# Kernel tuning notes

Hardware: AMD Instinct MI355X
Metric: run time of the kernel (lower is better)

## Reference

```python
import jax, jax.numpy as jnp
import numpy as np


def fwht(x):
    """Unnormalized fast Walsh-Hadamard transform over a 1-D vector (len = power of 2).
    Matches the torch chunk/cat stage ordering (MSB-first butterfly)."""
    n = x.shape[0]
    ll = int(round(np.log2(n)))
    for ii in range(ll):
        x = x.reshape(2 ** ii, 2, -1)
        x = jnp.concatenate([x[:, :1] + x[:, 1:], x[:, :1] - x[:, 1:]], axis=1)
    return x.reshape(n)


@jax.custom_vjp
def fwht_ff(x):
    # mirrors torch FastWalshHadamard.apply: plain FWHT forward,
    # backward = FWHT(grad) / sqrt(n) (as defined in the original autograd Function)
    return fwht(x)

def _fwht_ff_fwd(x):
    scale = jnp.asarray(1.0 / np.sqrt(float(x.shape[0])), x.dtype)
    return fwht(x), scale

def _fwht_ff_bwd(scale, g):
    return (scale * fwht(g),)

fwht_ff.defvjp(_fwht_ff_fwd, _fwht_ff_bwd)


def fastfood(theta, BB, Pi, GG, DD):
    """Fastfood projection of theta (dim dd) to DD dims using fixed vars."""
    LL = BB.shape[0]
    dd = theta.shape[0]
    k = min(dd, LL)  # F.pad with negative pad truncates; replicate that
    xx = jnp.zeros(LL, theta.dtype).at[:k].set(theta[:k])
    m2 = fwht(BB * xx)          # H B x
    m4 = m2[Pi] * GG            # G Pi H B x
    m5 = fwht_ff(m4)            # H G Pi H B x
    divisor = jnp.sqrt(LL * jnp.sum(GG * GG))
    return m5[:DD] / (divisor * np.sqrt(float(DD) / LL))


def _mk_ff_vars(key, DD):
    ll = int(np.ceil(np.log2(DD)))
    LL = 2 ** ll
    k1, k2, k3 = jax.random.split(key, 3)
    BB = jax.random.randint(k1, (LL,), 0, 2).astype(jnp.float32) * 2.0 - 1.0
    Pi = jax.random.permutation(k2, LL).astype(jnp.int32)
    GG = jax.random.normal(k3, (LL,), dtype=jnp.float32)
    return BB, Pi, GG


D_IN, D_HID, D_OUT = 768, 3072, 768
INTRINSIC = 2048
BATCH = 256


def setup_inputs() -> dict:
    key = jax.random.key(0)
    ks = jax.random.split(key, 12)
    x = jax.random.normal(ks[0], (BATCH, D_IN), dtype=jnp.float32)
    # original initializes intrinsic_parameter to zeros; use small randn so the
    # Fastfood path contributes non-trivially to the output for testing
    theta = jax.random.normal(ks[1], (INTRINSIC,), dtype=jnp.float32) * 0.01
    init_W1 = jax.random.normal(ks[2], (D_HID, D_IN), dtype=jnp.float32) * 0.02
    init_b1 = jax.random.normal(ks[3], (D_HID,), dtype=jnp.float32) * 0.02
    init_W2 = jax.random.normal(ks[4], (D_OUT, D_HID), dtype=jnp.float32) * 0.02
    init_b2 = jax.random.normal(ks[5], (D_OUT,), dtype=jnp.float32) * 0.02
    BB_W1, Pi_W1, GG_W1 = _mk_ff_vars(ks[6], D_HID * D_IN)
    BB_b1, Pi_b1, GG_b1 = _mk_ff_vars(ks[7], D_HID)
    BB_W2, Pi_W2, GG_W2 = _mk_ff_vars(ks[8], D_OUT * D_HID)
    BB_b2, Pi_b2, GG_b2 = _mk_ff_vars(ks[9], D_OUT)
    return {
        'x': x, 'theta': theta,
        'init_W1': init_W1, 'init_b1': init_b1, 'init_W2': init_W2, 'init_b2': init_b2,
        'BB_W1': BB_W1, 'Pi_W1': Pi_W1, 'GG_W1': GG_W1,
        'BB_b1': BB_b1, 'Pi_b1': Pi_b1, 'GG_b1': GG_b1,
        'BB_W2': BB_W2, 'Pi_W2': Pi_W2, 'GG_W2': GG_W2,
        'BB_b2': BB_b2, 'Pi_b2': Pi_b2, 'GG_b2': GG_b2,
    }


def reference(x, theta, init_W1, init_b1, init_W2, init_b2,
              BB_W1, Pi_W1, GG_W1, BB_b1, Pi_b1, GG_b1,
              BB_W2, Pi_W2, GG_W2, BB_b2, Pi_b2, GG_b2):
    # param = initial_value + fastfood(theta) for every wrapped parameter
    W1 = init_W1 + fastfood(theta, BB_W1, Pi_W1, GG_W1, init_W1.size).reshape(init_W1.shape)
    b1 = init_b1 + fastfood(theta, BB_b1, Pi_b1, GG_b1, init_b1.size)
    W2 = init_W2 + fastfood(theta, BB_W2, Pi_W2, GG_W2, init_W2.size).reshape(init_W2.shape)
    b2 = init_b2 + fastfood(theta, BB_b2, Pi_b2, GG_b2, init_b2.size)
    # wrapped module forward: Linear -> ReLU -> Linear
    h = jax.nn.relu(x @ W1.T + b1)
    return h @ W2.T + b2
```

## Files before the change

kernel.cpp:

```cpp
#include <hip/hip_runtime.h>
#include <hip/hip_bf16.h>

typedef __attribute__((ext_vector_type(8))) short bf16x8;
typedef __attribute__((ext_vector_type(8))) unsigned short u16x8;
typedef __attribute__((ext_vector_type(4))) float f32x4;

template <int N, int S>
__device__ __forceinline__ void reg_fwht(float* v) {
#pragma unroll
  for (int h = 1; h < N; h <<= 1)
#pragma unroll
    for (int g = 0; g < N; g += 2 * h)
#pragma unroll
      for (int j = 0; j < h; ++j) {
        float a = v[(g + j) * S], b = v[(g + j + h) * S];
        v[(g + j) * S] = a + b;
        v[(g + j + h) * S] = a - b;
      }
}

__device__ __forceinline__ unsigned short f2bf(float f) {
  unsigned u = __float_as_uint(f);
  unsigned r = (u + 0x7fff + ((u >> 16) & 1)) >> 16;
  return (unsigned short)r;
}

__device__ __forceinline__ void lds_fwht(float* s, int n, int tid, int T) {
  for (int h = 1; h < n; h <<= 1) {
    __syncthreads();
    for (int t = tid; t < (n >> 1); t += T) {
      int i0 = ((t & ~(h - 1)) << 1) | (t & (h - 1));
      int i1 = i0 + h;
      float a = s[i0], b = s[i1];
      s[i0] = a + b;
      s[i1] = a - b;
    }
  }
  __syncthreads();
}

__device__ __forceinline__ void fwht2048_block(float w[8], float* pad,
                                               float* dst, int t) {
  reg_fwht<8, 1>(w);
#pragma unroll
  for (int j = 0; j < 8; ++j) {
    int i = t + 256 * j;
    pad[i + 4 * (i >> 5)] = w[j];
  }
  __syncthreads();
  {
    int base = 8 * t + 4 * (t >> 2);
    float4 a = *(float4*)(pad + base);
    float4 b = *(float4*)(pad + base + 4);
    float u[8] = {a.x, a.y, a.z, a.w, b.x, b.y, b.z, b.w};
    reg_fwht<8, 1>(u);
    *(float4*)(pad + base) = make_float4(u[0], u[1], u[2], u[3]);
    *(float4*)(pad + base + 4) = make_float4(u[4], u[5], u[6], u[7]);
  }
  __syncthreads();
  {
    int b0 = (t & 7) + 64 * (t >> 3);
    float u[8];
#pragma unroll
    for (int j = 0; j < 8; ++j) {
      int i = b0 + 8 * j;
      u[j] = pad[i + 4 * (i >> 5)];
    }
    reg_fwht<8, 1>(u);
#pragma unroll
    for (int j = 0; j < 8; ++j) {
      int i = b0 + 8 * j;
      pad[i + 4 * (i >> 5)] = u[j];
    }
  }
  __syncthreads();
#pragma unroll
  for (int g = 0; g < 2; ++g) {
    int b0 = (t & 63) + 256 * ((g << 2) | (t >> 6));
    float u[4];
#pragma unroll
    for (int j = 0; j < 4; ++j) {
      int i = b0 + 64 * j;
      u[j] = pad[i + 4 * (i >> 5)];
    }
    reg_fwht<4, 1>(u);
#pragma unroll
    for (int j = 0; j < 4; ++j) dst[b0 + 64 * j] = u[j];
  }
  __syncthreads();
}

__global__ __launch_bounds__(256) void k_pre(
    const float* __restrict__ theta, const float* __restrict__ BB0,
    const float* __restrict__ BB1, float* __restrict__ m2s,
    const float* __restrict__ x, __hip_bfloat16* __restrict__ xb) {
  __shared__ __align__(16) float pad[2304];
  int b = blockIdx.x, t = threadIdx.x;
  if (b < 2) {
    const float* BB = b ? BB1 : BB0;
    float w[8];
#pragma unroll
    for (int j = 0; j < 8; ++j) {
      int i = t + 256 * j;
      w[j] = BB[i] * theta[i];
    }
    fwht2048_block(w, pad, m2s + b * 2048, t);
  } else {
    int id0 = (b - 2) * 256 + t;
#pragma unroll
    for (int it = 0; it < 2; ++it) {
      int id = id0 + it * 24576;
      float4 xv = ((const float4*)x)[id];
      ushort4 o;
      o.x = f2bf(xv.x);
      o.y = f2bf(xv.y);
      o.z = f2bf(xv.z);
      o.w = f2bf(xv.w);
      ((ushort4*)xb)[id] = o;
    }
  }
}

#define LLW 4194304

__global__ __launch_bounds__(256) void k_front(
    const int* __restrict__ Pi1, const float* __restrict__ GG1,
    const int* __restrict__ Pi2, const float* __restrict__ GG2,
    const float* __restrict__ m2s, unsigned short* __restrict__ m4b,
    float* __restrict__ partial, const float* __restrict__ theta,
    const float* __restrict__ BBb1, const int* __restrict__ Pib1,
    const float* __restrict__ GGb1, const float* __restrict__ ib1,
    float* __restrict__ b1w, const float* __restrict__ BBb2,
    const int* __restrict__ Pib2, const float* __restrict__ GGb2,
    const float* __restrict__ ib2, float* __restrict__ b2w) {
  __shared__ __align__(16) float s[9216];
  __shared__ float red[4];
  int b = blockIdx.x, t = threadIdx.x;

  if (b >= 2) {
    int bb = b - 2;
    int pipe = bb >> 9, chunk = bb & 511;
    const int* Pi = pipe ? Pi2 : Pi1;
    const float* GG = pipe ? GG2 : GG1;
    const float* mm = m2s + pipe * 2048;
    for (int u = t; u < 512; u += 256) ((float4*)s)[u] = ((const float4*)mm)[u];
    __syncthreads();

    long base = (long)chunk * 8192;
    const int4* p4 = (const int4*)(Pi + base);
    const float4* g4 = (const float4*)(GG + base);
    float v[32];
    float lsum = 0.f;
#pragma unroll
    for (int j = 0; j < 8; ++j) {
      int4 p = p4[t + j * 256];
      float4 g = g4[t + j * 256];
      lsum += g.x * g.x + g.y * g.y + g.z * g.z + g.w * g.w;
      v[j * 4 + 0] = s[p.x & 2047] * g.x;
      v[j * 4 + 1] = s[p.y & 2047] * g.y;
      v[j * 4 + 2] = s[p.z & 2047] * g.z;
      v[j * 4 + 3] = s[p.w & 2047] * g.w;
    }
    for (int off = 32; off; off >>= 1) lsum += __shfl_down(lsum, off, 64);
    if ((t & 63) == 0) red[t >> 6] = lsum;

#pragma unroll
    for (int e = 0; e < 4; ++e) reg_fwht<8, 4>(v + e);

    __syncthreads();
    if (t == 0) partial[pipe * 512 + chunk] = red[0] + red[1] + red[2] + red[3];

#pragma unroll
    for (int j = 0; j < 8; ++j) {
      int A = t * 4 + 4 * (t >> 3) + j * 1152;
      *(float4*)(s + A) =
          make_float4(v[j * 4], v[j * 4 + 1], v[j * 4 + 2], v[j * 4 + 3]);
    }
    __syncthreads();
    {
      int b0 = (t & 31) + (t >> 5) * 1024;
      float w[32];
#pragma unroll
      for (int j2 = 0; j2 < 32; ++j2) {
        int i = b0 + j2 * 32;
        w[j2] = s[i + 4 * (i >> 5)];
      }
      reg_fwht<32, 1>(w);
#pragma unroll
      for (int j2 = 0; j2 < 32; ++j2) {
        int i = b0 + j2 * 32;
        s[i + 4 * (i >> 5)] = w[j2];
      }
    }
    __syncthreads();
#pragma unroll
    for (int q = 0; q < 8; ++q) {
      float4 r = *(const float4*)(s + t * 36 + q * 4);
      v[q * 4 + 0] = r.x;
      v[q * 4 + 1] = r.y;
      v[q * 4 + 2] = r.z;
      v[q * 4 + 3] = r.w;
    }
    reg_fwht<32, 1>(v);
    unsigned short* o = m4b + (long)pipe * LLW + base + t * 32;
#pragma unroll
    for (int q = 0; q < 4; ++q) {
      u16x8 pk;
#pragma unroll
      for (int e = 0; e < 8; ++e) pk[e] = f2bf(v[q * 8 + e]);
      *(u16x8*)(o + q * 8) = pk;
    }
  } else if (b == 0) {
    float* tabd = s + 6144;
    float w[8];
#pragma unroll
    for (int j = 0; j < 8; ++j) {
      int i = t + 256 * j;
      w[j] = BBb1[i] * theta[i];
    }
    fwht2048_block(w, s, tabd, t);

    float w16[16];
    float lsum = 0.f;
#pragma unroll
    for (int j = 0; j < 16; ++j) {
      int i = t + 256 * j;
      float g = GGb1[i];
      lsum += g * g;
      w16[j] = tabd[Pib1[i] & 2047] * g;
    }
    reg_fwht<16, 1>(w16);
#pragma unroll
    for (int j = 0; j < 16; ++j) {
      int i = t + 256 * j;
      s[i + 4 * (i >> 5)] = w16[j];
    }
    for (int off = 32; off; off >>= 1) lsum += __shfl_down(lsum, off, 64);
    if ((t & 63) == 0) s[4608 + (t >> 6)] = lsum;
    __syncthreads();
    float S = s[4608] + s[4609] + s[4610] + s[4611];
    {
      int base16 = 16 * t + 4 * (t >> 1);
      float u[16];
#pragma unroll
      for (int q = 0; q < 4; ++q) {
        float4 r = *(float4*)(s + base16 + q * 4);
        u[q * 4 + 0] = r.x;
        u[q * 4 + 1] = r.y;
        u[q * 4 + 2] = r.z;
        u[q * 4 + 3] = r.w;
      }
      reg_fwht<16, 1>(u);
#pragma unroll
      for (int q = 0; q < 4; ++q)
        *(float4*)(s + base16 + q * 4) =
            make_float4(u[q * 4], u[q * 4 + 1], u[q * 4 + 2], u[q * 4 + 3]);
    }
    __syncthreads();
    {
      float scale = 1.0f / sqrtf(S * 3072.0f);
      int b0 = (t & 15) + 256 * (t >> 4);
      float u[16];
#pragma unroll
      for (int j = 0; j < 16; ++j) {
        int i = b0 + 16 * j;
        u[j] = s[i + 4 * (i >> 5)];
      }
      reg_fwht<16, 1>(u);
#pragma unroll
      for (int j = 0; j < 16; ++j) {
        int i = b0 + 16 * j;
        if (i < 3072) b1w[i] = ib1[i] + u[j] * scale;
      }
    }
  } else {
    float* tab2 = s;
    float* m42 = s + 1024;
    for (int i = t; i < 1024; i += 256) tab2[i] = BBb2[i] * theta[i];
    lds_fwht(tab2, 1024, t, 256);
    float lsum = 0.f;
    for (int i = t; i < 1024; i += 256) {
      float g = GGb2[i];
      lsum += g * g;
      m42[i] = tab2[Pib2[i] & 1023] * g;
    }
    for (int off = 32; off; off >>= 1) lsum += __shfl_down(lsum, off, 64);
    if ((t & 63) == 0) s[2048 + (t >> 6)] = lsum;
    lds_fwht(m42, 1024, t, 256);
    float S = s[2048] + s[2049] + s[2050] + s[2051];
    float scale = 1.0f / sqrtf(S * 768.0f);
    for (int i = t; i < 768; i += 256) b2w[i] = ib2[i] + m42[i] * scale;
  }
}

__global__ __launch_bounds__(256) void k_f2c(
    const unsigned short* __restrict__ m4b, const float* __restrict__ iW1,
    const float* __restrict__ iW2, const float* __restrict__ partial,
    __hip_bfloat16* __restrict__ W1b, __hip_bfloat16* __restrict__ W2b) {
  __shared__ __align__(16) float s[10480];
  __shared__ float red[4];
  int b = blockIdx.x, t = threadIdx.x;
  int pipe = b >> 9;
  int l0 = (b & 511) * 16;
  const unsigned short* mp = m4b + (long)pipe * LLW;
  const float* initW = pipe ? iW2 : iW1;
  unsigned short* outW = (unsigned short*)(pipe ? W2b : W1b);

  {
    float ps = partial[pipe * 512 + t] + partial[pipe * 512 + 256 + t];
    for (int off = 32; off; off >>= 1) ps += __shfl_down(ps, off, 64);
    if ((t & 63) == 0) red[t >> 6] = ps;
  }

#pragma unroll
  for (int u = 0; u < 4; ++u) {
    int idx = t + u * 256;
    int r = idx >> 1, h8 = (idx & 1) * 8;
    u16x8 raw = *(const u16x8*)(mp + (long)r * 8192 + l0 + h8);
    float* dp = s + r * 20 + (r >> 5) * 16 + h8;
    float4 f0, f1v;
    f0.x = __uint_as_float((unsigned)raw[0] << 16);
    f0.y = __uint_as_float((unsigned)raw[1] << 16);
    f0.z = __uint_as_float((unsigned)raw[2] << 16);
    f0.w = __uint_as_float((unsigned)raw[3] << 16);
    f1v.x = __uint_as_float((unsigned)raw[4] << 16);
    f1v.y = __uint_as_float((unsigned)raw[5] << 16);
    f1v.z = __uint_as_float((unsigned)raw[6] << 16);
    f1v.w = __uint_as_float((unsigned)raw[7] << 16);
    *(float4*)dp = f0;
    *(float4*)(dp + 4) = f1v;
  }
  __syncthreads();

  {
    int c = t & 15, rg = t >> 4;
    float w[32];
#pragma unroll
    for (int j = 0; j < 32; ++j) {
      int r = rg * 32 + j;
      w[j] = s[r * 20 + (r >> 5) * 16 + c];
    }
    reg_fwht<32, 1>(w);
#pragma unroll
    for (int j = 0; j < 32; ++j) {
      int r = rg * 32 + j;
      s[r * 20 + (r >> 5) * 16 + c] = w[j];
    }
  }
  __syncthreads();

  {
    int c = t & 15;
    float w[32];
#pragma unroll
    for (int k = 0; k < 2; ++k) {
      int b0 = (t >> 4) * 2 + k;
#pragma unroll
      for (int j4 = 0; j4 < 16; ++j4) {
        int r = b0 + 32 * j4;
        w[k * 16 + j4] = s[r * 20 + (r >> 5) * 16 + c];
      }
      reg_fwht<16, 1>(w + k * 16);
#pragma unroll
      for (int j4 = 0; j4 < 16; ++j4) {
        int r = b0 + 32 * j4;
        s[r * 20 + (r >> 5) * 16 + c] = w[k * 16 + j4];
      }
    }
  }
  __syncthreads();

  float S = red[0] + red[1] + red[2] + red[3];
  float scale = 1.0f / sqrtf(S * 2359296.0f);
#pragma unroll
  for (int u = 0; u < 5; ++u) {
    int idx = t + u * 256;
    if (idx < 1152) {
      int r = idx >> 2, c4 = (idx & 3) * 4;
      const float* sp = s + r * 20 + (r >> 5) * 16 + c4;
      long gi = (long)r * 8192 + l0 + c4;
      float4 iv = *(const float4*)(initW + gi);
      ushort4 pk;
      pk.x = f2bf(iv.x + sp[0] * scale);
      pk.y = f2bf(iv.y + sp[1] * scale);
      pk.z = f2bf(iv.z + sp[2] * scale);
      pk.w = f2bf(iv.w + sp[3] * scale);
      *(ushort4*)(outW + gi) = pk;
    }
  }
}

template <int NACC, int KCH, bool RELU, bool OUT_BF16>
__global__ __launch_bounds__(256) void k_gemm(
    const __hip_bfloat16* __restrict__ A, const __hip_bfloat16* __restrict__ B,
    const float* __restrict__ bias, void* __restrict__ C, int M, int N, int K) {
  int wid = blockIdx.x * 4 + (threadIdx.x >> 6);
  int lane = threadIdx.x & 63;
  int ntiles = N / (16 * NACC);
  int mt = wid / ntiles, nt = wid % ntiles;
  if (mt * 16 >= M) return;
  int ml = lane & 15;
  int q = lane >> 4;
  const short* As = (const short*)A;
  const short* Bs = (const short*)B;
  long arow = (long)(mt * 16 + ml) * K + q * 8;
  int KH = K / KCH;
  f32x4 acc[KCH][NACC] = {};
  for (int k = 0; k < KH; k += 32) {
#pragma unroll
    for (int c = 0; c < KCH; ++c) {
      bf16x8 av = *(const bf16x8*)(As + arow + k + c * KH);
#pragma unroll
      for (int a = 0; a < NACC; ++a) {
        int n = nt * 16 * NACC + a * 16 + ml;
        bf16x8 bv = *(const bf16x8*)(Bs + (long)n * K + q * 8 + k + c * KH);
        acc[c][a] =
            __builtin_amdgcn_mfma_f32_16x16x32_bf16(av, bv, acc[c][a], 0, 0, 0);
      }
    }
  }
#pragma unroll
  for (int a = 0; a < NACC; ++a) {
    int n = nt * 16 * NACC + a * 16 + ml;
    float bv = bias[n];
#pragma unroll
    for (int r = 0; r < 4; ++r) {
      float vv = bv;
#pragma unroll
      for (int c = 0; c < KCH; ++c) vv += acc[c][a][r];
      int mm = mt * 16 + q * 4 + r;
      if (RELU) vv = fmaxf(vv, 0.f);
      if (OUT_BF16)
        ((__hip_bfloat16*)C)[(long)mm * N + n] = __float2bfloat16(vv);
      else
        ((float*)C)[(long)mm * N + n] = vv;
    }
  }
}

#define OFF_PART 0
#define OFF_M2S 4096
#define OFF_M4B (OFF_M2S + 16384)
#define OFF_W1B (OFF_M4B + 2 * LLW * 2)
#define OFF_W2B (OFF_W1B + 4718592)
#define OFF_HB (OFF_W2B + 4718592)
#define OFF_XB (OFF_HB + 1572864)
#define OFF_B1 (OFF_XB + 393216)
#define OFF_B2 (OFF_B1 + 12288)

extern "C" void kernel_launch(void* const* d_in, const int* in_sizes, int n_in,
                              void* d_out, int out_size, void* d_ws,
                              size_t ws_size, hipStream_t stream) {
  const float* x = (const float*)d_in[0];
  const float* theta = (const float*)d_in[1];
  const float* iW1 = (const float*)d_in[2];
  const float* ib1 = (const float*)d_in[3];
  const float* iW2 = (const float*)d_in[4];
  const float* ib2 = (const float*)d_in[5];
  const float* BB_W1 = (const float*)d_in[6];
  const int* Pi_W1 = (const int*)d_in[7];
  const float* GG_W1 = (const float*)d_in[8];
  const float* BB_b1 = (const float*)d_in[9];
  const int* Pi_b1 = (const int*)d_in[10];
  const float* GG_b1 = (const float*)d_in[11];
  const float* BB_W2 = (const float*)d_in[12];
  const int* Pi_W2 = (const int*)d_in[13];
  const float* GG_W2 = (const float*)d_in[14];
  const float* BB_b2 = (const float*)d_in[15];
  const int* Pi_b2 = (const int*)d_in[16];
  const float* GG_b2 = (const float*)d_in[17];

  char* ws = (char*)d_ws;
  float* partial = (float*)(ws + OFF_PART);
  float* m2s = (float*)(ws + OFF_M2S);
  unsigned short* m4b = (unsigned short*)(ws + OFF_M4B);
  __hip_bfloat16* W1b = (__hip_bfloat16*)(ws + OFF_W1B);
  __hip_bfloat16* W2b = (__hip_bfloat16*)(ws + OFF_W2B);
  __hip_bfloat16* hb = (__hip_bfloat16*)(ws + OFF_HB);
  __hip_bfloat16* xb = (__hip_bfloat16*)(ws + OFF_XB);
  float* b1w = (float*)(ws + OFF_B1);
  float* b2w = (float*)(ws + OFF_B2);

  k_pre<<<98, 256, 0, stream>>>(theta, BB_W1, BB_W2, m2s, x, xb);
  k_front<<<1026, 256, 0, stream>>>(Pi_W1, GG_W1, Pi_W2, GG_W2, m2s, m4b,
                                    partial, theta, BB_b1, Pi_b1, GG_b1, ib1,
                                    b1w, BB_b2, Pi_b2, GG_b2, ib2, b2w);
  k_f2c<<<1024, 256, 0, stream>>>(m4b, iW1, iW2, partial, W1b, W2b);
  k_gemm<2, 1, true, true><<<384, 256, 0, stream>>>(xb, W1b, b1w, hb, 256,
                                                    3072, 768);
  k_gemm<1, 2, false, false><<<192, 256, 0, stream>>>(hb, W2b, b2w, d_out, 256,
                                                      768, 3072);
}
```

Before: 226.9 us.

## Transpose m4b intermediate layout and split-K GEMMs across waves with LDS reduction

The front kernel now writes the bf16 FWHT intermediate in a layout where each f2c block reads one contiguous 8192-element segment, and f2c remaps block indices to match. This turns strided gathers into coalesced reads at the cost of strided writes in the producer. Both GEMMs switch from per-wave in-register K chunking to split-K across waves within a block, reduced through shared memory. This doubles or quadruples the number of blocks for more parallelism, but adds a __syncthreads and LDS traffic.

```diff
diff --git a/kernel.cpp b/kernel.cpp
--- a/kernel.cpp
+++ b/kernel.cpp
@@ -202,13 +202,14 @@
       v[q * 4 + 3] = r.w;
     }
     reg_fwht<32, 1>(v);
-    unsigned short* o = m4b + (long)pipe * LLW + base + t * 32;
+    unsigned short* o = m4b + (long)pipe * LLW;
+    long a0 = (long)(2 * t) * 8192 + (long)chunk * 16;
 #pragma unroll
     for (int q = 0; q < 4; ++q) {
       u16x8 pk;
 #pragma unroll
       for (int e = 0; e < 8; ++e) pk[e] = f2bf(v[q * 8 + e]);
-      *(u16x8*)(o + q * 8) = pk;
+      *(u16x8*)(o + a0 + (q >> 1) * 8192 + (q & 1) * 8) = pk;
     }
   } else if (b == 0) {
     float* tabd = s + 6144;
@@ -301,8 +302,10 @@
   __shared__ float red[4];
   int b = blockIdx.x, t = threadIdx.x;
   int pipe = b >> 9;
-  int l0 = (b & 511) * 16;
-  const unsigned short* mp = m4b + (long)pipe * LLW;
+  int lb = b & 511;
+  int g = ((lb & 7) << 6) | (lb >> 3);
+  int l0 = g * 16;
+  const unsigned short* mp = m4b + (long)pipe * LLW + (long)g * 8192;
   const float* initW = pipe ? iW2 : iW1;
   unsigned short* outW = (unsigned short*)(pipe ? W2b : W1b);
 
@@ -313,11 +316,10 @@
   }
 
 #pragma unroll
-  for (int u = 0; u < 4; ++u) {
-    int idx = t + u * 256;
-    int r = idx >> 1, h8 = (idx & 1) * 8;
-    u16x8 raw = *(const u16x8*)(mp + (long)r * 8192 + l0 + h8);
-    float* dp = s + r * 20 + (r >> 5) * 16 + h8;
+  for (int q = 0; q < 4; ++q) {
+    u16x8 raw = *(const u16x8*)(mp + t * 32 + q * 8);
+    int r = 2 * t + (q >> 1), cb = (q & 1) * 8;
+    float* dp = s + r * 20 + (r >> 5) * 16 + cb;
     float4 f0, f1v;
     f0.x = __uint_as_float((unsigned)raw[0] << 16);
     f0.y = __uint_as_float((unsigned)raw[1] << 16);
@@ -390,50 +392,56 @@
   }
 }
 
-template <int NACC, int KCH, bool RELU, bool OUT_BF16>
+template <int NACC, int SPLITK, bool RELU, bool OUT_BF16>
 __global__ __launch_bounds__(256) void k_gemm(
     const __hip_bfloat16* __restrict__ A, const __hip_bfloat16* __restrict__ B,
     const float* __restrict__ bias, void* __restrict__ C, int M, int N, int K) {
-  int wid = blockIdx.x * 4 + (threadIdx.x >> 6);
-  int lane = threadIdx.x & 63;
+  __shared__ float red[4 * NACC * 320];
+  int wave = threadIdx.x >> 6, lane = threadIdx.x & 63;
+  int tileid = blockIdx.x * (4 / SPLITK) + wave / SPLITK;
+  int sk = wave % SPLITK;
   int ntiles = N / (16 * NACC);
-  int mt = wid / ntiles, nt = wid % ntiles;
-  if (mt * 16 >= M) return;
+  int mt = tileid / ntiles, nt = tileid % ntiles;
   int ml = lane & 15;
   int q = lane >> 4;
   const short* As = (const short*)A;
   const short* Bs = (const short*)B;
   long arow = (long)(mt * 16 + ml) * K + q * 8;
-  int KH = K / KCH;
-  f32x4 acc[KCH][NACC] = {};
-  for (int k = 0; k < KH; k += 32) {
-#pragma unroll
-    for (int c = 0; c < KCH; ++c) {
-      bf16x8 av = *(const bf16x8*)(As + arow + k + c * KH);
-#pragma unroll
-      for (int a = 0; a < NACC; ++a) {
-        int n = nt * 16 * NACC + a * 16 + ml;
-        bf16x8 bv = *(const bf16x8*)(Bs + (long)n * K + q * 8 + k + c * KH);
-        acc[c][a] =
-            __builtin_amdgcn_mfma_f32_16x16x32_bf16(av, bv, acc[c][a], 0, 0, 0);
-      }
-    }
-  }
-#pragma unroll
-  for (int a = 0; a < NACC; ++a) {
-    int n = nt * 16 * NACC + a * 16 + ml;
-    float bv = bias[n];
-#pragma unroll
-    for (int r = 0; r < 4; ++r) {
-      float vv = bv;
-#pragma unroll
-      for (int c = 0; c < KCH; ++c) vv += acc[c][a][r];
-      int mm = mt * 16 + q * 4 + r;
-      if (RELU) vv = fmaxf(vv, 0.f);
-      if (OUT_BF16)
-        ((__hip_bfloat16*)C)[(long)mm * N + n] = __float2bfloat16(vv);
-      else
-        ((float*)C)[(long)mm * N + n] = vv;
+  int KS = K / SPLITK, k0 = sk * KS;
+  f32x4 acc[NACC] = {};
+  for (int k = k0; k < k0 + KS; k += 32) {
+    bf16x8 av = *(const bf16x8*)(As + arow + k);
+#pragma unroll
+    for (int a = 0; a < NACC; ++a) {
+      int n = nt * 16 * NACC + a * 16 + ml;
+      bf16x8 bv = *(const bf16x8*)(Bs + (long)n * K + q * 8 + k);
+      acc[a] = __builtin_amdgcn_mfma_f32_16x16x32_bf16(av, bv, acc[a], 0, 0, 0);
+    }
+  }
+#pragma unroll
+  for (int a = 0; a < NACC; ++a)
+#pragma unroll
+    for (int r = 0; r < 4; ++r)
+      red[(wave * NACC + a) * 320 + lane * 5 + r] = acc[a][r];
+  __syncthreads();
+  if (sk == 0) {
+#pragma unroll
+    for (int a = 0; a < NACC; ++a) {
+      int n = nt * 16 * NACC + a * 16 + ml;
+      float bv = bias[n];
+#pragma unroll
+      for (int r = 0; r < 4; ++r) {
+        float vv = bv;
+#pragma unroll
+        for (int j = 0; j < SPLITK; ++j)
+          vv += red[((wave + j) * NACC + a) * 320 + lane * 5 + r];
+        int mm = mt * 16 + q * 4 + r;
+        if (RELU) vv = fmaxf(vv, 0.f);
+        if (OUT_BF16)
+          ((__hip_bfloat16*)C)[(long)mm * N + n] = __float2bfloat16(vv);
+        else
+          ((float*)C)[(long)mm * N + n] = vv;
+      }
     }
   }
 }
@@ -486,8 +494,8 @@
                                     partial, theta, BB_b1, Pi_b1, GG_b1, ib1,
                                     b1w, BB_b2, Pi_b2, GG_b2, ib2, b2w);
   k_f2c<<<1024, 256, 0, stream>>>(m4b, iW1, iW2, partial, W1b, W2b);
-  k_gemm<2, 1, true, true><<<384, 256, 0, stream>>>(xb, W1b, b1w, hb, 256,
+  k_gemm<2, 2, true, true><<<768, 256, 0, stream>>>(xb, W1b, b1w, hb, 256,
                                                     3072, 768);
-  k_gemm<1, 2, false, false><<<192, 256, 0, stream>>>(hb, W2b, b2w, d_out, 256,
+  k_gemm<1, 4, false, false><<<768, 256, 0, stream>>>(hb, W2b, b2w, d_out, 256,
                                                       768, 3072);
 }
```

Measured after the change: 217.1 us, median of 2. -4.3%, faster.
